# Kernel tuning notes

Hardware: AMD Instinct MI355X
Metric: run time of the kernel (lower is better)

Reference implementation:

```python
import jax, jax.numpy as jnp
from jax import lax
import numpy as np

NUM_CLASSES = 7
EDGE_LO, EDGE_HI = 2, 7  # edge_classes = [2,3,4,5,6]
FOCAL_W, DICE_W, BOUND_W, TOPO_W = 0.3, 0.3, 0.2, 0.2
GAMMA = 2.0


def _dwconv(x, k):
    # depthwise 'same' conv with identical spatial kernel per channel
    C = x.shape[1]
    kern = jnp.broadcast_to(k[None, None], (C, 1) + k.shape)
    return lax.conv_general_dilated(
        x, kern, (1, 1), 'SAME',
        dimension_numbers=('NCHW', 'OIHW', 'NCHW'),
        feature_group_count=C)


def setup_inputs() -> dict:
    key = jax.random.key(0)
    k1, k2 = jax.random.split(key)
    logits = jax.random.normal(k1, (8, NUM_CLASSES, 512, 512), dtype=jnp.float32)
    targets = jax.random.randint(k2, (8, 512, 512), 0, NUM_CLASSES, dtype=jnp.int32)
    class_weights = jnp.ones((NUM_CLASSES,), dtype=jnp.float32)
    return {"logits": logits, "targets": targets, "class_weights": class_weights}


def reference(logits, targets, class_weights):
    C = logits.shape[1]
    logp = jax.nn.log_softmax(logits, axis=1)          # [B,C,H,W]
    probs = jnp.exp(logp)
    onehot = (targets[:, None, :, :] == jnp.arange(C)[None, :, None, None]).astype(logits.dtype)

    # ---- Focal loss (weighted CE, pt from the *weighted* CE as in torch code) ----
    nll = -jnp.take_along_axis(logp, targets[:, None].astype(jnp.int32), axis=1)[:, 0]  # [B,H,W]
    ce = class_weights[targets] * nll
    pt = jnp.exp(-ce)
    loss_focal = jnp.mean((1.0 - pt) ** GAMMA * ce)

    # ---- Dice loss (per class, global sums) ----
    inter = jnp.sum(probs * onehot, axis=(0, 2, 3))    # [C]
    union = jnp.sum(probs, axis=(0, 2, 3)) + jnp.sum(onehot, axis=(0, 2, 3))
    loss_dice = jnp.mean(1.0 - (2.0 * inter + 1e-6) / (union + 1e-6))

    # ---- Boundary loss ----
    lap = jnp.array([[0., 1., 0.], [1., -4., 1.], [0., 1., 0.]], dtype=jnp.float32)
    boundary = (jnp.abs(_dwconv(onehot, lap)) > 0).astype(jnp.float32)
    region = _dwconv(boundary, jnp.ones((5, 5), jnp.float32))
    bweight = 1.0 + 4.0 * (region > 0).astype(jnp.float32)
    bce = -onehot * jnp.log(probs + 1e-7) - (1.0 - onehot) * jnp.log(1.0 - probs + 1e-7)
    # sum_c mean_{B,H,W}(bce*w)/C == mean over [B,C,H,W]
    loss_boundary = jnp.mean(bce * bweight)

    # ---- Topology loss (edge classes 2..6) ----
    avg = jnp.ones((3, 3), jnp.float32) / 9.0
    pc = _dwconv(probs[:, EDGE_LO:EDGE_HI], avg)
    tc = _dwconv(onehot[:, EDGE_LO:EDGE_HI], avg)
    diff = jnp.abs(pc - tc)
    mask = onehot[:, EDGE_LO:EDGE_HI]
    msum = jnp.sum(mask, axis=(0, 2, 3))               # [5]
    num = jnp.sum(diff * mask, axis=(0, 2, 3))
    per_cls = jnp.where(msum >= 1.0, num / jnp.maximum(msum, 1.0), 0.0)
    loss_topo = jnp.sum(per_cls) / float(EDGE_HI - EDGE_LO)

    return FOCAL_W * loss_focal + DICE_W * loss_dice + BOUND_W * loss_boundary + TOPO_W * loss_topo
```

## Files before the change

kernel.cpp:

```cpp
#include <hip/hip_runtime.h>
#include <hip/hip_fp16.h>

#define BB 8
#define CC 7
#define HH 512
#define WW 512
#define HW (HH*WW)
#define NBLK 1024


__device__ __forceinline__ float dpp_red(float v) {
#define STEP(ctrl) v += __int_as_float(__builtin_amdgcn_update_dpp(0, __float_as_int(v), ctrl, 0xF, 0xF, true))
    STEP(0x111); STEP(0x112); STEP(0x114); STEP(0x118);
    STEP(0x142); STEP(0x143);
#undef STEP
    return v;
}

__device__ __forceinline__ void softmax7x4(float4 a[7]) {
#pragma unroll
    for (int c = 0; c < 7; c++) {
        a[c].x = __expf(a[c].x); a[c].y = __expf(a[c].y);
        a[c].z = __expf(a[c].z); a[c].w = __expf(a[c].w);
    }
    float4 se = a[0];
#pragma unroll
    for (int c = 1; c < 7; c++) { se.x += a[c].x; se.y += a[c].y; se.z += a[c].z; se.w += a[c].w; }
    float ix = 1.f/se.x, iy = 1.f/se.y, iz = 1.f/se.z, iw = 1.f/se.w;
#pragma unroll
    for (int c = 0; c < 7; c++) { a[c].x *= ix; a[c].y *= iy; a[c].z *= iz; a[c].w *= iw; }
}

__device__ __forceinline__ void write_planes(unsigned short* sp, const float4 a[7], int r, int cI) {
#pragma unroll
    for (int c = 2; c < 7; c++) {
        unsigned lo = (unsigned)__half_as_ushort(__float2half_rn(a[c].x))
                    | ((unsigned)__half_as_ushort(__float2half_rn(a[c].y)) << 16);
        unsigned hi = (unsigned)__half_as_ushort(__float2half_rn(a[c].z))
                    | ((unsigned)__half_as_ushort(__float2half_rn(a[c].w)) << 16);
        *(uint2*)&sp[(c - 2) * 1360 + r * 40 + cI * 4] = make_uint2(lo, hi);
    }
}

__device__ __forceinline__ void pixel_body(const float pr[7], int t, unsigned rmv,
                                           const unsigned short* sp, const unsigned char* st,
                                           const float* sw, int cy, int cx,
                                           float& accF, float& accB,
                                           float* sumP, float* inter, float* cnt, float* num) {
    float p_t = pr[0];
#pragma unroll
    for (int c = 1; c < 7; c++) p_t = (t == c) ? pr[c] : p_t;
    float ce = sw[t] * (-__logf(p_t));
    float ptv = __expf(-ce);
    float om = 1.0f - ptv;
    accF += om * om * ce;

    float prodA = 1.0f, prodB = 1.0f;
#pragma unroll
    for (int c = 0; c < 7; c++) {
        float p = pr[c];
        bool is = (c == t);
        sumP[c] += p;
        if (is) { inter[c] += p; cnt[c] += 1.0f; }
        float arg = is ? (p + 1e-7f) : (1.0f - p + 1e-7f);
        prodA *= arg;
        prodB *= ((rmv >> c) & 1u) ? arg : 1.0f;
    }
    accB -= __logf(prodA) + 4.0f * __logf(prodB);

    if ((unsigned)(t - 2) < 5u) {
        const unsigned short* pl = sp + (t - 2) * 1360;
        int base = (cy + 1) * 40 + (cx + 4);
        int sb = (cy + 3) * 40 + (cx + 4);
        float s = 0.f;
#pragma unroll
        for (int dy = -1; dy <= 1; dy++) {
#pragma unroll
            for (int dx = -1; dx <= 1; dx++) {
                float pn = __half2float(__ushort_as_half(pl[base + dy * 40 + dx]));
                s += pn - ((st[sb + dy * 40 + dx] == t) ? 1.0f : 0.0f);
            }
        }
        float val = fabsf(s) * (1.0f / 9.0f);
#pragma unroll
        for (int q = 0; q < 5; q++) num[q] += (t == q + 2) ? val : 0.f;
    }
}

__device__ __forceinline__ void load_tgt(int tid, int gy0, int gx0, const int* tg,
                                         int4& tv0, bool& v0, int4& tv1, bool& v1) {
    {
        int r = tid / 10, cI = tid - r * 10;
        int y = gy0 - 3 + r, xs = gx0 - 4 + cI * 4;
        v0 = ((unsigned)y < HH) && ((unsigned)xs < WW);
        size_t off = v0 ? ((size_t)y * WW + xs) : 0;
        tv0 = *(const int4*)(tg + off);
    }
    {
        int g = tid + 256; int gc = (g < 380) ? g : 0;
        int r = gc / 10, cI = gc - r * 10;
        int y = gy0 - 3 + r, xs = gx0 - 4 + cI * 4;
        v1 = (g < 380) && ((unsigned)y < HH) && ((unsigned)xs < WW);
        size_t off = v1 ? ((size_t)y * WW + xs) : 0;
        tv1 = *(const int4*)(tg + off);
    }
}

__device__ __forceinline__ void store_st(int tid, int4 tv0, bool v0, int4 tv1, bool v1,
                                         unsigned char* st) {
    {
        int r = tid / 10, cI = tid - r * 10;
        unsigned w = v0 ? ((unsigned)tv0.x | ((unsigned)tv0.y << 8) |
                           ((unsigned)tv0.z << 16) | ((unsigned)tv0.w << 24))
                        : 0xFFFFFFFFu;
        *(unsigned*)&st[r * 40 + cI * 4] = w;
    }
    if (tid + 256 < 380) {
        int g = tid + 256;
        int r = g / 10, cI = g - r * 10;
        unsigned w = v1 ? ((unsigned)tv1.x | ((unsigned)tv1.y << 8) |
                           ((unsigned)tv1.z << 16) | ((unsigned)tv1.w << 24))
                        : 0xFFFFFFFFu;
        *(unsigned*)&st[r * 40 + cI * 4] = w;
    }
}

__device__ __forceinline__ void load_int(int tid, int gy0, int gx0, const float* lg, float4 aI[7]) {
    const int rI = 1 + (tid >> 3), cII = 1 + (tid & 7);
    const float* p0 = lg + (size_t)(gy0 - 1 + rI) * WW + (gx0 - 4 + cII * 4);
#pragma unroll
    for (int c = 0; c < 7; c++) aI[c] = *(const float4*)(p0 + (size_t)c * HW);
}

__device__ __forceinline__ void load_halo(int tid, int gy0, int gx0, const float* lg,
                                          float4 aH[7], bool& hvld, int& hr, int& hc) {
    hvld = false; hr = 0; hc = 0;
    if (tid < 84) {
        if (tid < 10)      { hr = 0;  hc = tid; }
        else if (tid < 20) { hr = 33; hc = tid - 10; }
        else { int e = tid - 20; hr = 1 + (e >> 1); hc = (e & 1) ? 9 : 0; }
        int y = gy0 - 1 + hr, xs = gx0 - 4 + hc * 4;
        hvld = ((unsigned)y < HH) && ((unsigned)xs < WW);
        size_t off = hvld ? ((size_t)y * WW + xs) : 0;
        const float* p0 = lg + off;
#pragma unroll
        for (int c = 0; c < 7; c++) aH[c] = *(const float4*)(p0 + (size_t)c * HW);
    }
}

__device__ __forceinline__ void halo_softmax_store(int tid, float4 aH[7], bool hvld,
                                                   int hr, int hc, unsigned short* sp) {
    if (tid < 84) {
        if (hvld) {
            softmax7x4(aH);
        } else {
#pragma unroll
            for (int c = 0; c < 7; c++) aH[c] = make_float4(0.f, 0.f, 0.f, 0.f);
        }
        write_planes(sp, aH, hr, hc);
    }
}

__device__ __forceinline__ void build_masks(int tid, int gy0, int gx0,
                                            const unsigned char* st, unsigned char* bm,
                                            unsigned char* hm, unsigned char* rm) {
    for (int p = tid; p < 1296; p += 256) {
        int by = p / 36, bx = p - by * 36;
        int y = gy0 - 2 + by, x = gx0 - 2 + bx;
        unsigned bits = 0;
        if ((unsigned)y < HH && (unsigned)x < WW) {
            int si = (by + 1) * 40 + (bx + 2);
            int t = st[si];
            unsigned orm = 0; int nfirst = -1, same = 1, ninb = 0;
            int n;
            n = st[si - 40]; if (n != 255) { orm |= 1u << n; if (nfirst < 0) nfirst = n; else same &= (n == nfirst); ninb++; }
            n = st[si + 40]; if (n != 255) { orm |= 1u << n; if (nfirst < 0) nfirst = n; else same &= (n == nfirst); ninb++; }
            n = st[si - 1];  if (n != 255) { orm |= 1u << n; if (nfirst < 0) nfirst = n; else same &= (n == nfirst); ninb++; }
            n = st[si + 1];  if (n != 255) { orm |= 1u << n; if (nfirst < 0) nfirst = n; else same &= (n == nfirst); ninb++; }
            unsigned andm = (ninb == 4 && same) ? (1u << nfirst) : 0u;
            unsigned cbit = 1u << t;
            bits = (orm & ~cbit) | (cbit & ~andm);
        }
        bm[p] = (unsigned char)bits;
    }
    __syncthreads();
    for (int p = tid; p < 1152; p += 256) {
        int hy = p >> 5, hx = p & 31;
        const unsigned char* r = &bm[hy * 36 + hx];
        hm[p] = (unsigned char)(r[0] | r[1] | r[2] | r[3] | r[4]);
    }
    __syncthreads();
#pragma unroll
    for (int k = 0; k < 4; k++) {
        int p = tid + k * 256;
        const unsigned char* hc2 = &hm[(p >> 5) * 32 + (p & 31)];
        rm[p] = (unsigned char)(hc2[0] | hc2[32] | hc2[64] | hc2[96] | hc2[128]);
    }
    __syncthreads();
}

__device__ __forceinline__ void phase_b(int tid, const float4 aI[7],
                                        const unsigned short* sp, const unsigned char* st,
                                        const unsigned char* rm, const float* sw,
                                        float& accF, float& accB,
                                        float* sumP, float* inter, float* cnt, float* num) {
    const int cy = tid >> 3, cxb = (tid & 7) * 4;
    unsigned rmv4 = *(const unsigned*)&rm[cy * 32 + cxb];
    unsigned t4 = *(const unsigned*)&st[(cy + 3) * 40 + cxb + 4];
    {
        float pr[7] = {aI[0].x, aI[1].x, aI[2].x, aI[3].x, aI[4].x, aI[5].x, aI[6].x};
        pixel_body(pr, (int)(t4 & 255u), rmv4 & 255u, sp, st, sw, cy, cxb + 0,
                   accF, accB, sumP, inter, cnt, num);
    }
    {
        float pr[7] = {aI[0].y, aI[1].y, aI[2].y, aI[3].y, aI[4].y, aI[5].y, aI[6].y};
        pixel_body(pr, (int)((t4 >> 8) & 255u), (rmv4 >> 8) & 255u, sp, st, sw, cy, cxb + 1,
                   accF, accB, sumP, inter, cnt, num);
    }
    {
        float pr[7] = {aI[0].z, aI[1].z, aI[2].z, aI[3].z, aI[4].z, aI[5].z, aI[6].z};
        pixel_body(pr, (int)((t4 >> 16) & 255u), (rmv4 >> 16) & 255u, sp, st, sw, cy, cxb + 2,
                   accF, accB, sumP, inter, cnt, num);
    }
    {
        float pr[7] = {aI[0].w, aI[1].w, aI[2].w, aI[3].w, aI[4].w, aI[5].w, aI[6].w};
        pixel_body(pr, (int)((t4 >> 24) & 255u), (rmv4 >> 24) & 255u, sp, st, sw, cy, cxb + 3,
                   accF, accB, sumP, inter, cnt, num);
    }
}

__global__ __launch_bounds__(256) void main_kernel(const float* __restrict__ logits,
                                                   const int* __restrict__ tgt,
                                                   const float* __restrict__ cw,
                                                   float* __restrict__ part) {
    __shared__ unsigned short sp[5 * 1360];
    __shared__ unsigned char st[40 * 38];
    __shared__ unsigned char bm[36 * 36];
    __shared__ unsigned char hm[36 * 32];
    __shared__ unsigned char rm[1024];
    __shared__ float sw[8];
    __shared__ float sred[112];

    const int tid = threadIdx.x;
    const int b = blockIdx.z;
    const int gx0 = blockIdx.x * 32;
    const int gy0a = blockIdx.y * 64;
    const int gy0b = blockIdx.y * 64 + 32;
    if (tid < 7) sw[tid] = cw[tid];

    const float* lg = logits + (size_t)b * CC * HW;
    const int* tg = tgt + (size_t)b * HW;

    float accF = 0.f, accB = 0.f;
    float sumP[7] = {0,0,0,0,0,0,0};
    float inter[7] = {0,0,0,0,0,0,0};
    float cnt[7] = {0,0,0,0,0,0,0};
    float num[5] = {0,0,0,0,0};

    int4 tv0, tv1; bool v0, v1;
    load_tgt(tid, gy0a, gx0, tg, tv0, v0, tv1, v1);
    float4 aI[7];
    load_int(tid, gy0a, gx0, lg, aI);
    float4 aH[7]; bool hvld; int hr, hc;
    load_halo(tid, gy0a, gx0, lg, aH, hvld, hr, hc);

    store_st(tid, tv0, v0, tv1, v1, st);
    {
        const int rI = 1 + (tid >> 3), cII = 1 + (tid & 7);
        softmax7x4(aI);
        write_planes(sp, aI, rI, cII);
    }
    halo_softmax_store(tid, aH, hvld, hr, hc, sp);

    int4 u0, u1; bool w0, w1;
    load_tgt(tid, gy0b, gx0, tg, u0, w0, u1, w1);
    float4 aJ[7];
    load_int(tid, gy0b, gx0, lg, aJ);

    __syncthreads();
    build_masks(tid, gy0a, gx0, st, bm, hm, rm);
    phase_b(tid, aI, sp, st, rm, sw, accF, accB, sumP, inter, cnt, num);
    __syncthreads();

    store_st(tid, u0, w0, u1, w1, st);
    {
        const int rI = 1 + (tid >> 3), cII = 1 + (tid & 7);
        softmax7x4(aJ);
        write_planes(sp, aJ, rI, cII);
    }
    load_halo(tid, gy0b, gx0, lg, aH, hvld, hr, hc);
    halo_softmax_store(tid, aH, hvld, hr, hc, sp);

    __syncthreads();
    build_masks(tid, gy0b, gx0, st, bm, hm, rm);
    phase_b(tid, aJ, sp, st, rm, sw, accF, accB, sumP, inter, cnt, num);

    float vals[28];
    vals[0] = accF; vals[1] = accB;
#pragma unroll
    for (int c = 0; c < 7; c++) { vals[2+c] = sumP[c]; vals[9+c] = inter[c]; vals[16+c] = cnt[c]; }
#pragma unroll
    for (int j = 0; j < 5; j++) vals[23+j] = num[j];

    const int lane = tid & 63, wid = tid >> 6;
#pragma unroll
    for (int i = 0; i < 28; i++) {
        float v = dpp_red(vals[i]);
        if (lane == 63) sred[wid * 28 + i] = v;
    }
    __syncthreads();
    if (tid < 28) {
        float s = sred[tid] + sred[28 + tid] + sred[56 + tid] + sred[84 + tid];
        int bid = (blockIdx.z * gridDim.y + blockIdx.y) * gridDim.x + blockIdx.x;
        part[tid * NBLK + bid] = s;
    }
}

__global__ __launch_bounds__(1024) void reduce_kernel(const float* __restrict__ part,
                                                      float* __restrict__ out) {
    __shared__ double fin[28];
    const int tid = threadIdx.x;
    const int w = tid >> 6, lane = tid & 63;
    for (int j = w; j < 28; j += 16) {
        double s = 0.0;
#pragma unroll
        for (int k = 0; k < NBLK / 64; k++) s += (double)part[j * NBLK + lane + k * 64];
#pragma unroll
        for (int o = 32; o > 0; o >>= 1) s += __shfl_down(s, o, 64);
        if (lane == 0) fin[j] = s;
    }
    __syncthreads();
    if (tid == 0) {
        double focal = fin[0] / (double)((size_t)BB * HW);
        double bound = fin[1] / (double)((size_t)BB * CC * HW);
        double dice = 0.0;
#pragma unroll
        for (int c = 0; c < 7; c++) {
            double uni = fin[2 + c] + fin[16 + c];
            dice += 1.0 - (2.0 * fin[9 + c] + 1e-6) / (uni + 1e-6);
        }
        dice *= (1.0 / 7.0);
        double topo = 0.0;
#pragma unroll
        for (int j = 0; j < 5; j++) {
            double ms = fin[18 + j];
            double nm = fin[23 + j];
            topo += (ms >= 1.0) ? nm / fmax(ms, 1.0) : 0.0;
        }
        topo *= (1.0 / 5.0);
        out[0] = (float)(0.3 * focal + 0.3 * dice + 0.2 * bound + 0.2 * topo);
    }
}

extern "C" void kernel_launch(void* const* d_in, const int* in_sizes, int n_in,
                              void* d_out, int out_size, void* d_ws, size_t ws_size,
                              hipStream_t stream) {
    const float* logits = (const float*)d_in[0];
    const int* tgt = (const int*)d_in[1];
    const float* cw = (const float*)d_in[2];
    float* out = (float*)d_out;
    float* part = (float*)d_ws;

    dim3 grid(WW / 32, HH / 64, BB);
    main_kernel<<<grid, 256, 0, stream>>>(logits, tgt, cw, part);
    reduce_kernel<<<1, 1024, 0, stream>>>(part, out);
}
```

Baseline: 135.8 us.

## Trim halo loads to needed columns, prefetch second halo, remap blocks across XCDs

Halo loading for logits and targets now fetches only the single columns and rows the stencils need, instead of whole float4/int4 groups that are mostly unused. Side halo pixels get a scalar softmax that writes only the edge-class planes. The second tile's halo is loaded early, before the first tile is processed, so its latency overlaps with that work. Block IDs are remapped so that neighbouring tiles land on the same XCD, aiming for better L2 reuse of the overlapping halos, at the cost of more registers for aH2 and scattered scalar loads.

```diff
diff --git a/kernel.cpp b/kernel.cpp
--- a/kernel.cpp
+++ b/kernel.cpp
@@ -88,76 +88,118 @@
 }
 
 __device__ __forceinline__ void load_tgt(int tid, int gy0, int gx0, const int* tg,
-                                         int4& tv0, bool& v0, int4& tv1, bool& v1) {
-    {
-        int r = tid / 10, cI = tid - r * 10;
-        int y = gy0 - 3 + r, xs = gx0 - 4 + cI * 4;
-        v0 = ((unsigned)y < HH) && ((unsigned)xs < WW);
-        size_t off = v0 ? ((size_t)y * WW + xs) : 0;
+                                         int4& tv0, int4& tv1, int& tvH) {
+    {
+        int r = tid >> 3, j4 = (tid & 7) * 4;
+        int y = gy0 - 3 + r;
+        size_t off = ((unsigned)y < HH) ? ((size_t)y * WW + gx0 + j4) : 0;
         tv0 = *(const int4*)(tg + off);
     }
     {
-        int g = tid + 256; int gc = (g < 380) ? g : 0;
-        int r = gc / 10, cI = gc - r * 10;
-        int y = gy0 - 3 + r, xs = gx0 - 4 + cI * 4;
-        v1 = (g < 380) && ((unsigned)y < HH) && ((unsigned)xs < WW);
-        size_t off = v1 ? ((size_t)y * WW + xs) : 0;
+        int g = tid + 256; int gc = (g < 304) ? g : 256;
+        int r = gc >> 3, j4 = (gc & 7) * 4;
+        int y = gy0 - 3 + r;
+        size_t off = ((g < 304) && (unsigned)y < HH) ? ((size_t)y * WW + gx0 + j4) : 0;
         tv1 = *(const int4*)(tg + off);
     }
-}
-
-__device__ __forceinline__ void store_st(int tid, int4 tv0, bool v0, int4 tv1, bool v1,
-                                         unsigned char* st) {
-    {
-        int r = tid / 10, cI = tid - r * 10;
-        unsigned w = v0 ? ((unsigned)tv0.x | ((unsigned)tv0.y << 8) |
-                           ((unsigned)tv0.z << 16) | ((unsigned)tv0.w << 24))
-                        : 0xFFFFFFFFu;
-        *(unsigned*)&st[r * 40 + cI * 4] = w;
-    }
-    if (tid + 256 < 380) {
+    tvH = 255;
+    if (tid < 228) {
+        int r = tid / 6, k = tid - r * 6;
+        int c_st = (k < 3) ? (1 + k) : (33 + k);
+        int x = gx0 + c_st - 4;
+        int y = gy0 - 3 + r;
+        if ((unsigned)y < HH && (unsigned)x < WW) tvH = tg[(size_t)y * WW + x];
+    }
+}
+
+__device__ __forceinline__ void store_st(int tid, int gy0, const int4& tv0, const int4& tv1,
+                                         int tvH, unsigned char* st) {
+    {
+        int r = tid >> 3, j4 = (tid & 7) * 4;
+        int y = gy0 - 3 + r;
+        unsigned w = ((unsigned)y < HH)
+            ? ((unsigned)tv0.x | ((unsigned)tv0.y << 8) | ((unsigned)tv0.z << 16) | ((unsigned)tv0.w << 24))
+            : 0xFFFFFFFFu;
+        *(unsigned*)&st[r * 40 + 4 + j4] = w;
+    }
+    if (tid < 48) {
         int g = tid + 256;
-        int r = g / 10, cI = g - r * 10;
-        unsigned w = v1 ? ((unsigned)tv1.x | ((unsigned)tv1.y << 8) |
-                           ((unsigned)tv1.z << 16) | ((unsigned)tv1.w << 24))
-                        : 0xFFFFFFFFu;
-        *(unsigned*)&st[r * 40 + cI * 4] = w;
+        int r = g >> 3, j4 = (g & 7) * 4;
+        int y = gy0 - 3 + r;
+        unsigned w = ((unsigned)y < HH)
+            ? ((unsigned)tv1.x | ((unsigned)tv1.y << 8) | ((unsigned)tv1.z << 16) | ((unsigned)tv1.w << 24))
+            : 0xFFFFFFFFu;
+        *(unsigned*)&st[r * 40 + 4 + j4] = w;
+    }
+    if (tid < 228) {
+        int r = tid / 6, k = tid - r * 6;
+        int c_st = (k < 3) ? (1 + k) : (33 + k);
+        st[r * 40 + c_st] = (unsigned char)tvH;
     }
 }
 
 __device__ __forceinline__ void load_int(int tid, int gy0, int gx0, const float* lg, float4 aI[7]) {
-    const int rI = 1 + (tid >> 3), cII = 1 + (tid & 7);
-    const float* p0 = lg + (size_t)(gy0 - 1 + rI) * WW + (gx0 - 4 + cII * 4);
+    const int rI = 1 + (tid >> 3);
+    const float* p0 = lg + (size_t)(gy0 - 1 + rI) * WW + (gx0 + (tid & 7) * 4);
 #pragma unroll
     for (int c = 0; c < 7; c++) aI[c] = *(const float4*)(p0 + (size_t)c * HW);
 }
 
-__device__ __forceinline__ void load_halo(int tid, int gy0, int gx0, const float* lg,
-                                          float4 aH[7], bool& hvld, int& hr, int& hc) {
-    hvld = false; hr = 0; hc = 0;
-    if (tid < 84) {
-        if (tid < 10)      { hr = 0;  hc = tid; }
-        else if (tid < 20) { hr = 33; hc = tid - 10; }
-        else { int e = tid - 20; hr = 1 + (e >> 1); hc = (e & 1) ? 9 : 0; }
-        int y = gy0 - 1 + hr, xs = gx0 - 4 + hc * 4;
-        hvld = ((unsigned)y < HH) && ((unsigned)xs < WW);
-        size_t off = hvld ? ((size_t)y * WW + xs) : 0;
-        const float* p0 = lg + off;
-#pragma unroll
-        for (int c = 0; c < 7; c++) aH[c] = *(const float4*)(p0 + (size_t)c * HW);
-    }
-}
-
-__device__ __forceinline__ void halo_softmax_store(int tid, float4 aH[7], bool hvld,
-                                                   int hr, int hc, unsigned short* sp) {
-    if (tid < 84) {
-        if (hvld) {
+__device__ __forceinline__ void load_halo(int tid, int gy0, int gx0, const float* lg, float4 aH[7]) {
+    if (tid < 16) {
+        int r = (tid >> 3) ? 33 : 0;
+        int g = tid & 7;
+        int y = gy0 - 1 + r;
+        if ((unsigned)y < HH) {
+            const float* p0 = lg + (size_t)y * WW + gx0 + g * 4;
+#pragma unroll
+            for (int c = 0; c < 7; c++) aH[c] = *(const float4*)(p0 + (size_t)c * HW);
+        }
+    } else if (tid < 84) {
+        int p = tid - 16;
+        int r = p >> 1;
+        int x = (p & 1) ? (gx0 + 32) : (gx0 - 1);
+        int y = gy0 - 1 + r;
+        if ((unsigned)y < HH && (unsigned)x < WW) {
+            const float* p0 = lg + (size_t)y * WW + x;
+#pragma unroll
+            for (int c = 0; c < 7; c++) aH[c].x = p0[(size_t)c * HW];
+        }
+    }
+}
+
+__device__ __forceinline__ void halo_softmax_store(int tid, int gy0, int gx0,
+                                                   float4 aH[7], unsigned short* sp) {
+    if (tid < 16) {
+        int r = (tid >> 3) ? 33 : 0;
+        int g = tid & 7;
+        int y = gy0 - 1 + r;
+        if ((unsigned)y < HH) {
             softmax7x4(aH);
         } else {
 #pragma unroll
             for (int c = 0; c < 7; c++) aH[c] = make_float4(0.f, 0.f, 0.f, 0.f);
         }
-        write_planes(sp, aH, hr, hc);
+        write_planes(sp, aH, r, 1 + g);
+    } else if (tid < 84) {
+        int p = tid - 16;
+        int r = p >> 1;
+        int side = p & 1;
+        int x = side ? (gx0 + 32) : (gx0 - 1);
+        int y = gy0 - 1 + r;
+        int col = side ? 36 : 3;
+        if ((unsigned)y < HH && (unsigned)x < WW) {
+            float e[7]; float se = 0.f;
+#pragma unroll
+            for (int c = 0; c < 7; c++) { e[c] = __expf(aH[c].x); se += e[c]; }
+            float inv = 1.0f / se;
+#pragma unroll
+            for (int c = 2; c < 7; c++)
+                sp[(c - 2) * 1360 + r * 40 + col] = __half_as_ushort(__float2half_rn(e[c] * inv));
+        } else {
+#pragma unroll
+            for (int c = 2; c < 7; c++) sp[(c - 2) * 1360 + r * 40 + col] = 0;
+        }
     }
 }
 
@@ -242,14 +284,16 @@
     __shared__ float sred[112];
 
     const int tid = threadIdx.x;
-    const int b = blockIdx.z;
-    const int gx0 = blockIdx.x * 32;
-    const int gy0a = blockIdx.y * 64;
-    const int gy0b = blockIdx.y * 64 + 32;
+    const int hw = (blockIdx.z * 8 + blockIdx.y) * 16 + blockIdx.x;
+    const int lb = (hw & 7) * 128 + (hw >> 3);
+    const int bx = lb & 15, byi = (lb >> 4) & 7, bz = lb >> 7;
+    const int gx0 = bx * 32;
+    const int gy0a = byi * 64;
+    const int gy0b = byi * 64 + 32;
     if (tid < 7) sw[tid] = cw[tid];
 
-    const float* lg = logits + (size_t)b * CC * HW;
-    const int* tg = tgt + (size_t)b * HW;
+    const float* lg = logits + (size_t)bz * CC * HW;
+    const int* tg = tgt + (size_t)bz * HW;
 
     float accF = 0.f, accB = 0.f;
     float sumP[7] = {0,0,0,0,0,0,0};
@@ -257,39 +301,40 @@
     float cnt[7] = {0,0,0,0,0,0,0};
     float num[5] = {0,0,0,0,0};
 
-    int4 tv0, tv1; bool v0, v1;
-    load_tgt(tid, gy0a, gx0, tg, tv0, v0, tv1, v1);
+    int4 tv0, tv1; int tvH;
+    load_tgt(tid, gy0a, gx0, tg, tv0, tv1, tvH);
     float4 aI[7];
     load_int(tid, gy0a, gx0, lg, aI);
-    float4 aH[7]; bool hvld; int hr, hc;
-    load_halo(tid, gy0a, gx0, lg, aH, hvld, hr, hc);
-
-    store_st(tid, tv0, v0, tv1, v1, st);
+    float4 aH[7];
+    load_halo(tid, gy0a, gx0, lg, aH);
+
+    store_st(tid, gy0a, tv0, tv1, tvH, st);
     {
         const int rI = 1 + (tid >> 3), cII = 1 + (tid & 7);
         softmax7x4(aI);
         write_planes(sp, aI, rI, cII);
     }
-    halo_softmax_store(tid, aH, hvld, hr, hc, sp);
-
-    int4 u0, u1; bool w0, w1;
-    load_tgt(tid, gy0b, gx0, tg, u0, w0, u1, w1);
+    halo_softmax_store(tid, gy0a, gx0, aH, sp);
+
+    int4 u0, u1; int uH;
+    load_tgt(tid, gy0b, gx0, tg, u0, u1, uH);
     float4 aJ[7];
     load_int(tid, gy0b, gx0, lg, aJ);
+    float4 aH2[7];
+    load_halo(tid, gy0b, gx0, lg, aH2);
 
     __syncthreads();
     build_masks(tid, gy0a, gx0, st, bm, hm, rm);
     phase_b(tid, aI, sp, st, rm, sw, accF, accB, sumP, inter, cnt, num);
     __syncthreads();
 
-    store_st(tid, u0, w0, u1, w1, st);
+    store_st(tid, gy0b, u0, u1, uH, st);
     {
         const int rI = 1 + (tid >> 3), cII = 1 + (tid & 7);
         softmax7x4(aJ);
         write_planes(sp, aJ, rI, cII);
     }
-    load_halo(tid, gy0b, gx0, lg, aH, hvld, hr, hc);
-    halo_softmax_store(tid, aH, hvld, hr, hc, sp);
+    halo_softmax_store(tid, gy0b, gx0, aH2, sp);
 
     __syncthreads();
     build_masks(tid, gy0b, gx0, st, bm, hm, rm);
@@ -311,8 +356,7 @@
     __syncthreads();
     if (tid < 28) {
         float s = sred[tid] + sred[28 + tid] + sred[56 + tid] + sred[84 + tid];
-        int bid = (blockIdx.z * gridDim.y + blockIdx.y) * gridDim.x + blockIdx.x;
-        part[tid * NBLK + bid] = s;
+        part[tid * NBLK + lb] = s;
     }
 }
 
```

After: 137.7 us. Within noise of the previous version (+1.4%).
